# Performance work log

Hardware: AMD Instinct MI355X
Metric: run time of the kernel (lower is better)

Reference implementation:

```python
import jax, jax.numpy as jnp
import numpy as np


def setup_inputs() -> dict:
    key = jax.random.key(0)
    k_y, k_cb = jax.random.split(key)
    B, C, H, W = 8, 192, 64, 64
    G, K = 8, 512
    d = C // G  # 24
    y = jax.random.normal(k_y, (B, C, H, W), dtype=jnp.float32)
    codebooks = jax.random.normal(k_cb, (G, K, d), dtype=jnp.float32)
    return {"y": y, "codebooks": codebooks}


def reference(y, codebooks):
    # y: [B, C, H, W]; codebooks: [G, K, d] with C == G*d
    B, C, H, W = y.shape
    G, K, d = codebooks.shape
    # split channels into G groups of dim d -> vectors at each spatial pos
    x = y.reshape(B, G, d, H, W).transpose(0, 3, 4, 1, 2)  # [B,H,W,G,d]
    x2 = jnp.sum(x * x, axis=-1, keepdims=True)            # [B,H,W,G,1]
    e2 = jnp.sum(codebooks * codebooks, axis=-1)           # [G,K]
    xe = jnp.einsum('bhwgd,gkd->bhwgk', x, codebooks)      # [B,H,W,G,K]
    dist = x2 - 2.0 * xe + e2                              # [B,H,W,G,K]
    idx = jnp.argmin(dist, axis=-1)                        # [B,H,W,G] int
    # gather quantized vectors per group (to_feather)
    q = codebooks[jnp.arange(G), idx]                      # [B,H,W,G,d]
    y_ba = q.transpose(0, 3, 4, 1, 2).reshape(B, C, H, W)  # [B,C,H,W]
    code_index = idx.transpose(0, 3, 1, 2)                 # [B,G,H,W]
    # straight-through estimator
    universal_ctx = y + jax.lax.stop_gradient(y_ba - y)
    return universal_ctx, y_ba, code_index[:, None]        # [B,1,G,H,W]
```

## Files before the change

### kernel.cpp

```cpp
#include <hip/hip_runtime.h>

#define B_   8
#define C_   192
#define HW_  4096
#define G_   8
#define K_   512
#define D_   24
#define CBSZ (K_ * D_)
#define THREADS 512
#define NBLOCKS 512

#define FRAG_HW    12288
#define E2_OFF_HW  12288
#define EL_OFF_HW  13312
#define IMG_HW     25600
#define WS_IMG_HW  13312
#define WS_EL_BASE (8 * WS_IMG_HW)
#define WS_BIG_BYTES ((8 * WS_IMG_HW + 8 * FRAG_HW) * 2)

typedef float  f32x4 __attribute__((ext_vector_type(4)));
typedef int    i32x4 __attribute__((ext_vector_type(4)));
typedef short  s16x8 __attribute__((ext_vector_type(8)));
typedef short  s16x4 __attribute__((ext_vector_type(4)));
typedef unsigned long long u64;

static __device__ __forceinline__ unsigned umin_(unsigned a, unsigned b){return a<b?a:b;}
static __device__ __forceinline__ unsigned umax_(unsigned a, unsigned b){return a>b?a:b;}
static __device__ __forceinline__ unsigned short f2bf(float x){
    unsigned u=__float_as_uint(x);
    return (unsigned short)((u + 0x7FFFu + ((u>>16)&1u))>>16);
}
static __device__ __forceinline__ float bf2f(unsigned short h){return __uint_as_float(((unsigned)h)<<16);}
static __device__ __forceinline__ int dec_id(unsigned idb){
    return (int)((idb & 0x1F0u) | ((idb & 3u) << 2) | ((idb >> 2) & 3u));
}

__global__ __launch_bounds__(256) void vq_stage(
    const float* __restrict__ cb, unsigned short* __restrict__ ws, int wr_el)
{
    const int g = blockIdx.x >> 3;
    const int s = blockIdx.x & 7;
    const int tid = threadIdx.x;
    const float* cbg = cb + g * CBSZ;
    unsigned short* img = ws + g * WS_IMG_HW;
    unsigned short* eli = ws + WS_EL_BASE + g * FRAG_HW;

    for (int i = tid; i < 384; i += 256) {
        int gi = s * 384 + i;
        f32x4 v = ((const f32x4*)cbg)[gi];
        int i4 = gi << 2;
        int n  = i4 / 24;
        int k0 = i4 - n * 24;
        int off = (n >> 4) * 384 + (((k0 >> 3) << 4) + (n & 15)) * 8 + (k0 & 7);
        s16x4 h, l;
        #pragma unroll
        for (int j = 0; j < 4; ++j) {
            unsigned short eh = f2bf(v[j]);
            h[j] = (short)eh;
            l[j] = (short)f2bf(v[j] - bf2f(eh));
        }
        *(s16x4*)(&img[off]) = h;
        if (wr_el) *(s16x4*)(&eli[off]) = l;
    }
    if (tid < 64) {
        int n = s * 64 + tid;
        const float* row = cbg + n * D_;
        double s0 = 0.0, s1 = 0.0;
        #pragma unroll
        for (int j = 0; j < D_; j += 2) {
            double v0 = (double)row[j], v1 = (double)row[j+1];
            s0 = fma(v0,v0,s0); s1 = fma(v1,v1,s1);
        }
        ((float*)(img + E2_OFF_HW))[n] = (float)(256.0 + s0 + s1);
    }
}

template<bool ELWS>
__global__ __launch_bounds__(THREADS, 4) void vq_main(
    const float* __restrict__ y, const float* __restrict__ cb,
    const unsigned short* __restrict__ ws, float* __restrict__ out)
{
    __shared__ __align__(16) unsigned short sB[IMG_HW];

    const int bid = blockIdx.x;
    const int g = bid & 7;
    const int blkg = bid >> 3;
    const int tid = threadIdx.x;
    const int wave = tid >> 6, lane = tid & 63;
    const int c = lane & 15, q = lane >> 4;

    const float* cbg = cb + g * CBSZ;

    {
        const char* src = (const char*)(ws + g * WS_IMG_HW);
        char* dst = (char*)sB;
        #pragma unroll
        for (int it = 0; it < 4; ++it) {
            int off = it * 8192 + tid * 16;
            if (off < 26624)
                *(i32x4*)(dst + off) = *(const i32x4*)(src + off);
        }
    }
    if (ELWS) {
        const char* src = (const char*)(ws + WS_EL_BASE + g * FRAG_HW);
        char* dst = (char*)(sB + EL_OFF_HW);
        #pragma unroll
        for (int it = 0; it < 3; ++it) {
            int off = it * 8192 + tid * 16;
            *(i32x4*)(dst + off) = *(const i32x4*)(src + off);
        }
    } else {
        #pragma unroll
        for (int it = 0; it < 6; ++it) {
            int gi = it * THREADS + tid;
            f32x4 v = ((const f32x4*)cbg)[gi];
            int i4 = gi << 2;
            int n  = i4 / 24;
            int k0 = i4 - n * 24;
            int off = (n >> 4) * 384 + (((k0 >> 3) << 4) + (n & 15)) * 8 + (k0 & 7);
            s16x4 l;
            #pragma unroll
            for (int j = 0; j < 4; ++j) {
                unsigned short eh = f2bf(v[j]);
                l[j] = (short)f2bf(v[j] - bf2f(eh));
            }
            *(s16x4*)(&sB[EL_OFF_HW + off]) = l;
        }
    }
    __syncthreads();

    float* out0 = out;
    float* out1 = out + B_*C_*HW_;
    float* out2 = out + 2*B_*C_*HW_;

    const unsigned short* aH = sB + (lane < 48 ? lane : lane - 48) * 8;
    const unsigned short* aL = aH + EL_OFF_HW;
    const f32x4* e2p = (const f32x4*)((const float*)(sB + E2_OFF_HW) + (q << 2));

    const int wsid = (blkg << 3) + wave;

    #pragma unroll 1
    for (int p = 0; p < 2; ++p) {
        const int tt0   = wsid + (p << 10);
        const int hw    = (tt0 & 255) << 4;
        const int bimg0 = tt0 >> 8;
        int ybase[2];
        ybase[0] = (bimg0*C_ + g*D_)*HW_ + hw;
        ybase[1] = ybase[0] + 2*C_*HW_;

        s16x8 Xh[2], Xl[2];
        #pragma unroll
        for (int ti = 0; ti < 2; ++ti) {
            unsigned hx[4], lx[4];
            if (q < 3) {
                const float* yq = y + ybase[ti] + (q*8)*HW_ + c;
                float xf[8];
                #pragma unroll
                for (int jj = 0; jj < 8; ++jj) xf[jj] = -2.0f * yq[jj*HW_];
                #pragma unroll
                for (int p2 = 0; p2 < 4; ++p2) {
                    float f0 = xf[2*p2], f1 = xf[2*p2+1];
                    unsigned u0 = __float_as_uint(f0), u1v = __float_as_uint(f1);
                    hx[p2] = (u1v & 0xFFFF0000u) | (u0 >> 16);
                    float l0 = f0 - __uint_as_float(u0 & 0xFFFF0000u);
                    float l1 = f1 - __uint_as_float(u1v & 0xFFFF0000u);
                    lx[p2] = (unsigned)f2bf(l0) | ((unsigned)f2bf(l1) << 16);
                }
            } else {
                hx[0]=0u; hx[1]=0u; hx[2]=0u; hx[3]=0u;
                lx[0]=0u; lx[1]=0u; lx[2]=0u; lx[3]=0u;
            }
            Xh[ti] = __builtin_bit_cast(s16x8, (i32x4){(int)hx[0],(int)hx[1],(int)hx[2],(int)hx[3]});
            Xl[ti] = __builtin_bit_cast(s16x8, (i32x4){(int)lx[0],(int)lx[1],(int)lx[2],(int)lx[3]});
        }

        unsigned b1a[2] = {~0u, ~0u}, b2a[2] = {~0u, ~0u}, b3a[2] = {~0u, ~0u};
        #pragma unroll 4
        for (int t = 0; t < 32; ++t) {
            s16x8 eh  = *(const s16x8*)(aH + t * 384);
            s16x8 el  = *(const s16x8*)(aL + t * 384);
            f32x4 e2v = e2p[t * 4];
            f32x4 a0 = __builtin_amdgcn_mfma_f32_16x16x32_bf16(eh, Xh[0], e2v, 0,0,0);
            a0       = __builtin_amdgcn_mfma_f32_16x16x32_bf16(eh, Xl[0], a0,  0,0,0);
            a0       = __builtin_amdgcn_mfma_f32_16x16x32_bf16(el, Xh[0], a0,  0,0,0);
            f32x4 a1 = __builtin_amdgcn_mfma_f32_16x16x32_bf16(eh, Xh[1], e2v, 0,0,0);
            a1       = __builtin_amdgcn_mfma_f32_16x16x32_bf16(eh, Xl[1], a1,  0,0,0);
            a1       = __builtin_amdgcn_mfma_f32_16x16x32_bf16(el, Xh[1], a1,  0,0,0);
            #pragma unroll
            for (int r = 0; r < 4; ++r) {
                const unsigned id7 = (unsigned)((t << 2) | r);
                {
                    unsigned key = (__float_as_uint(a0[r]) & 0xFFFFFF80u) + id7;
                    unsigned t3, t2;
                    asm("v_med3_u32 %0, %1, %2, %3" : "=v"(t3) : "v"(key), "v"(b2a[0]), "v"(b3a[0]));
                    asm("v_med3_u32 %0, %1, %2, %3" : "=v"(t2) : "v"(key), "v"(b1a[0]), "v"(b2a[0]));
                    b3a[0] = t3; b2a[0] = t2; b1a[0] = umin_(b1a[0], key);
                }
                {
                    unsigned key = (__float_as_uint(a1[r]) & 0xFFFFFF80u) + id7;
                    unsigned t3, t2;
                    asm("v_med3_u32 %0, %1, %2, %3" : "=v"(t3) : "v"(key), "v"(b2a[1]), "v"(b3a[1]));
                    asm("v_med3_u32 %0, %1, %2, %3" : "=v"(t2) : "v"(key), "v"(b1a[1]), "v"(b2a[1]));
                    b3a[1] = t3; b2a[1] = t2; b1a[1] = umin_(b1a[1], key);
                }
            }
        }

        #pragma unroll
        for (int ti = 0; ti < 2; ++ti) {
            unsigned b1 = (b1a[ti] << 2) | (unsigned)q;
            unsigned b2 = (b2a[ti] << 2) | (unsigned)q;
            unsigned b3 = (b3a[ti] << 2) | (unsigned)q;
            #pragma unroll
            for (int d = 16; d < 64; d <<= 1) {
                unsigned o1=__shfl_xor(b1,d,64), o2=__shfl_xor(b2,d,64), o3=__shfl_xor(b3,d,64);
                unsigned x = umax_(b1,o1);
                unsigned yv= umin_(b2,o2);
                unsigned w = umax_(b2,o2);
                unsigned z = umin_(b3,o3);
                b1 = umin_(b1,o1);
                b2 = umin_(x,yv);
                b3 = umin_(umax_(x,yv), umin_(w,z));
            }

            const int gap = (int)((b2 >> 9) - (b1 >> 9));
            int kwin;
            if (__ballot(gap < 8) == 0ull) {
                kwin = dec_id(b1 & 511u);
            } else {
                float xfr[8];
                if (q < 3) {
                    const float* yq = y + ybase[ti] + (q*8)*HW_ + c;
                    #pragma unroll
                    for (int jj = 0; jj < 8; ++jj) xfr[jj] = -2.0f * yq[jj*HW_];
                } else {
                    #pragma unroll
                    for (int jj = 0; jj < 8; ++jj) xfr[jj] = 0.0f;
                }
                double xd[8];
                #pragma unroll
                for (int jj = 0; jj < 8; ++jj) xd[jj] = (double)xfr[jj];
                const unsigned cands[3] = {b1, b2, b3};
                u64 bestk = ~0ull;
                #pragma unroll
                for (int ci = 0; ci < 3; ++ci) {
                    int kc = dec_id(cands[ci] & 511u);
                    double s = 0.0;
                    if (q < 3) {
                        const f32x4* ce4 = (const f32x4*)(cbg + kc*D_ + (q<<3));
                        float ef[8];
                        *(f32x4*)&ef[0] = ce4[0];
                        *(f32x4*)&ef[4] = ce4[1];
                        #pragma unroll
                        for (int jj = 0; jj < 8; ++jj) {
                            double ev = (double)ef[jj];
                            s = fma(ev, ev, s);
                            s = fma(xd[jj], ev, s);
                        }
                    }
                    s += __shfl_xor(s, 16, 64);
                    s += __shfl_xor(s, 32, 64);
                    s += 256.0;
                    u64 kk = (((u64)__double_as_longlong(s)) & ~0x1FFull) | (u64)kc;
                    bestk = kk < bestk ? kk : bestk;
                }
                kwin = (int)(bestk & 511ull);
            }

            const float* cw = cbg + kwin * D_;
            if (q < 3) {
                const f32x4* cw4 = (const f32x4*)(cw + (q<<3));
                float v[8];
                *(f32x4*)&v[0] = cw4[0];
                *(f32x4*)&v[4] = cw4[1];
                const int ob = ybase[ti] + (q*8)*HW_ + c;
                #pragma unroll
                for (int jj = 0; jj < 8; ++jj) {
                    out0[ob + jj*HW_] = v[jj];
                    out1[ob + jj*HW_] = v[jj];
                }
            }
            if (lane < 16) {
                const int bimg = bimg0 + 2*ti;
                out2[(bimg*G_ + g)*HW_ + hw + lane] = (float)kwin;
            }
        }
    }
}

extern "C" void kernel_launch(void* const* d_in, const int* in_sizes, int n_in,
                              void* d_out, int out_size, void* d_ws, size_t ws_size,
                              hipStream_t stream) {
    const float* y  = (const float*)d_in[0];
    const float* cb = (const float*)d_in[1];
    float* out = (float*)d_out;
    unsigned short* ws = (unsigned short*)d_ws;

    const bool big = ws_size >= (size_t)WS_BIG_BYTES;
    vq_stage<<<dim3(64), dim3(256), 0, stream>>>(cb, ws, big ? 1 : 0);
    if (big) vq_main<true ><<<dim3(NBLOCKS), dim3(THREADS), 0, stream>>>(y, cb, ws, out);
    else     vq_main<false><<<dim3(NBLOCKS), dim3(THREADS), 0, stream>>>(y, cb, ws, out);
}
```

Before: 113.9 us.

## Read low-part codebook fragments from global memory to halve LDS and double blocks

In the big-workspace path, the low-precision codebook fragments are no longer copied into shared memory and are instead read directly from the global workspace in the inner MFMA loop. This halves LDS per block, which allows launch bounds of 8 blocks per CU, and the grid doubles to 1024 blocks, each processing one tile pair instead of two. The aim is higher occupancy and less per-block staging. In exchange, the inner loop now issues global/L2 loads that may add latency, and register pressure is tighter under the stricter launch bound.

```diff
diff --git a/kernel.cpp b/kernel.cpp
--- a/kernel.cpp
+++ b/kernel.cpp
@@ -8,12 +8,10 @@
 #define D_   24
 #define CBSZ (K_ * D_)
 #define THREADS 512
-#define NBLOCKS 512
 
 #define FRAG_HW    12288
 #define E2_OFF_HW  12288
 #define EL_OFF_HW  13312
-#define IMG_HW     25600
 #define WS_IMG_HW  13312
 #define WS_EL_BASE (8 * WS_IMG_HW)
 #define WS_BIG_BYTES ((8 * WS_IMG_HW + 8 * FRAG_HW) * 2)
@@ -75,12 +73,14 @@
     }
 }
 
-template<bool ELWS>
-__global__ __launch_bounds__(THREADS, 4) void vq_main(
+template<bool ELG>
+__global__ __launch_bounds__(THREADS, ELG ? 8 : 4) void vq_main(
     const float* __restrict__ y, const float* __restrict__ cb,
     const unsigned short* __restrict__ ws, float* __restrict__ out)
 {
-    __shared__ __align__(16) unsigned short sB[IMG_HW];
+    constexpr int NW    = ELG ? 1024 : 512;
+    constexpr int NPAIR = ELG ? 1 : 2;
+    __shared__ __align__(16) unsigned short sB[ELG ? 13312 : 25600];
 
     const int bid = blockIdx.x;
     const int g = bid & 7;
@@ -101,15 +101,7 @@
                 *(i32x4*)(dst + off) = *(const i32x4*)(src + off);
         }
     }
-    if (ELWS) {
-        const char* src = (const char*)(ws + WS_EL_BASE + g * FRAG_HW);
-        char* dst = (char*)(sB + EL_OFF_HW);
-        #pragma unroll
-        for (int it = 0; it < 3; ++it) {
-            int off = it * 8192 + tid * 16;
-            *(i32x4*)(dst + off) = *(const i32x4*)(src + off);
-        }
-    } else {
+    if constexpr (!ELG) {
         #pragma unroll
         for (int it = 0; it < 6; ++it) {
             int gi = it * THREADS + tid;
@@ -133,20 +125,24 @@
     float* out1 = out + B_*C_*HW_;
     float* out2 = out + 2*B_*C_*HW_;
 
-    const unsigned short* aH = sB + (lane < 48 ? lane : lane - 48) * 8;
-    const unsigned short* aL = aH + EL_OFF_HW;
+    const int alias8 = (lane < 48 ? lane : lane - 48) * 8;
+    const unsigned short* aH = sB + alias8;
+    const unsigned short* aLg = ELG ? (ws + WS_EL_BASE + g * FRAG_HW + alias8)
+                                    : (const unsigned short*)nullptr;
+    const unsigned short* aLs = ELG ? (const unsigned short*)nullptr
+                                    : (sB + EL_OFF_HW + alias8);
     const f32x4* e2p = (const f32x4*)((const float*)(sB + E2_OFF_HW) + (q << 2));
 
     const int wsid = (blkg << 3) + wave;
 
     #pragma unroll 1
-    for (int p = 0; p < 2; ++p) {
-        const int tt0   = wsid + (p << 10);
+    for (int p = 0; p < NPAIR; ++p) {
+        const int tt0   = wsid + p * 2 * NW;
         const int hw    = (tt0 & 255) << 4;
         const int bimg0 = tt0 >> 8;
         int ybase[2];
         ybase[0] = (bimg0*C_ + g*D_)*HW_ + hw;
-        ybase[1] = ybase[0] + 2*C_*HW_;
+        ybase[1] = ybase[0] + (NW >> 8)*C_*HW_;
 
         s16x8 Xh[2], Xl[2];
         #pragma unroll
@@ -177,8 +173,10 @@
         unsigned b1a[2] = {~0u, ~0u}, b2a[2] = {~0u, ~0u}, b3a[2] = {~0u, ~0u};
         #pragma unroll 4
         for (int t = 0; t < 32; ++t) {
-            s16x8 eh  = *(const s16x8*)(aH + t * 384);
-            s16x8 el  = *(const s16x8*)(aL + t * 384);
+            s16x8 eh = *(const s16x8*)(aH + t * 384);
+            s16x8 el;
+            if constexpr (ELG) el = *(const s16x8*)(aLg + t * 384);
+            else               el = *(const s16x8*)(aLs + t * 384);
             f32x4 e2v = e2p[t * 4];
             f32x4 a0 = __builtin_amdgcn_mfma_f32_16x16x32_bf16(eh, Xh[0], e2v, 0,0,0);
             a0       = __builtin_amdgcn_mfma_f32_16x16x32_bf16(eh, Xl[0], a0,  0,0,0);
@@ -281,7 +279,7 @@
                 }
             }
             if (lane < 16) {
-                const int bimg = bimg0 + 2*ti;
+                const int bimg = bimg0 + (NW >> 8)*ti;
                 out2[(bimg*G_ + g)*HW_ + hw + lane] = (float)kwin;
             }
         }
@@ -298,6 +296,6 @@
 
     const bool big = ws_size >= (size_t)WS_BIG_BYTES;
     vq_stage<<<dim3(64), dim3(256), 0, stream>>>(cb, ws, big ? 1 : 0);
-    if (big) vq_main<true ><<<dim3(NBLOCKS), dim3(THREADS), 0, stream>>>(y, cb, ws, out);
-    else     vq_main<false><<<dim3(NBLOCKS), dim3(THREADS), 0, stream>>>(y, cb, ws, out);
-}
+    if (big) vq_main<true ><<<dim3(1024), dim3(THREADS), 0, stream>>>(y, cb, ws, out);
+    else     vq_main<false><<<dim3(512),  dim3(THREADS), 0, stream>>>(y, cb, ws, out);
+}
```

After: 113.2 us. Within noise of the previous version (-0.6%).

## Switch split-precision MFMA to fp16, double block size, single pass per wave

Applied to the files above, without the earlier changes.

Replaces the bf16 hi/lo split of codebook and inputs with an fp16 hi/lo split using packed round-toward-zero conversion, and uses f16 MFMA. The energy offset drops to 128, and the refinement test now also fires on small distances to guard fp16 precision. Blocks grow to 1024 threads, so each wave handles one tile pair instead of looping twice, and the workspace stores the full image, lo part included, contiguously per group. This aims for fewer conversion instructions, more waves per block, and cheaper staging loads, at the cost of fp16 range and precision risks and a possibly more frequent exact fallback.

```diff
diff --git a/kernel.cpp b/kernel.cpp
--- a/kernel.cpp
+++ b/kernel.cpp
@@ -7,43 +7,46 @@
 #define K_   512
 #define D_   24
 #define CBSZ (K_ * D_)
-#define THREADS 512
+#define THREADS 1024
 #define NBLOCKS 512
 
 #define FRAG_HW    12288
 #define E2_OFF_HW  12288
 #define EL_OFF_HW  13312
 #define IMG_HW     25600
-#define WS_IMG_HW  13312
-#define WS_EL_BASE (8 * WS_IMG_HW)
-#define WS_BIG_BYTES ((8 * WS_IMG_HW + 8 * FRAG_HW) * 2)
+#define WS_SMALL_HW 13312
+#define WS_BIG_BYTES (G_ * IMG_HW * 2)
 
 typedef float  f32x4 __attribute__((ext_vector_type(4)));
 typedef int    i32x4 __attribute__((ext_vector_type(4)));
 typedef short  s16x8 __attribute__((ext_vector_type(8)));
 typedef short  s16x4 __attribute__((ext_vector_type(4)));
+typedef _Float16 h16x8 __attribute__((ext_vector_type(8)));
 typedef unsigned long long u64;
 
 static __device__ __forceinline__ unsigned umin_(unsigned a, unsigned b){return a<b?a:b;}
 static __device__ __forceinline__ unsigned umax_(unsigned a, unsigned b){return a>b?a:b;}
-static __device__ __forceinline__ unsigned short f2bf(float x){
-    unsigned u=__float_as_uint(x);
-    return (unsigned short)((u + 0x7FFFu + ((u>>16)&1u))>>16);
-}
-static __device__ __forceinline__ float bf2f(unsigned short h){return __uint_as_float(((unsigned)h)<<16);}
 static __device__ __forceinline__ int dec_id(unsigned idb){
     return (int)((idb & 0x1F0u) | ((idb & 3u) << 2) | ((idb >> 2) & 3u));
 }
+static __device__ __forceinline__ unsigned pkrtz(float a, float b){
+    return __builtin_bit_cast(unsigned, __builtin_amdgcn_cvt_pkrtz(a, b));
+}
+static __device__ __forceinline__ float lo16f(unsigned w){
+    return (float)__builtin_bit_cast(_Float16, (unsigned short)(w & 0xFFFFu));
+}
+static __device__ __forceinline__ float hi16f(unsigned w){
+    return (float)__builtin_bit_cast(_Float16, (unsigned short)(w >> 16));
+}
 
 __global__ __launch_bounds__(256) void vq_stage(
-    const float* __restrict__ cb, unsigned short* __restrict__ ws, int wr_el)
+    const float* __restrict__ cb, unsigned short* __restrict__ ws, int big)
 {
     const int g = blockIdx.x >> 3;
     const int s = blockIdx.x & 7;
     const int tid = threadIdx.x;
     const float* cbg = cb + g * CBSZ;
-    unsigned short* img = ws + g * WS_IMG_HW;
-    unsigned short* eli = ws + WS_EL_BASE + g * FRAG_HW;
+    unsigned short* img = ws + g * (big ? IMG_HW : WS_SMALL_HW);
 
     for (int i = tid; i < 384; i += 256) {
         int gi = s * 384 + i;
@@ -55,12 +58,13 @@
         s16x4 h, l;
         #pragma unroll
         for (int j = 0; j < 4; ++j) {
-            unsigned short eh = f2bf(v[j]);
-            h[j] = (short)eh;
-            l[j] = (short)f2bf(v[j] - bf2f(eh));
+            _Float16 eh = (_Float16)v[j];
+            _Float16 el = (_Float16)(v[j] - (float)eh);
+            h[j] = __builtin_bit_cast(short, eh);
+            l[j] = __builtin_bit_cast(short, el);
         }
         *(s16x4*)(&img[off]) = h;
-        if (wr_el) *(s16x4*)(&eli[off]) = l;
+        if (big) *(s16x4*)(&img[EL_OFF_HW + off]) = l;
     }
     if (tid < 64) {
         int n = s * 64 + tid;
@@ -71,12 +75,12 @@
             double v0 = (double)row[j], v1 = (double)row[j+1];
             s0 = fma(v0,v0,s0); s1 = fma(v1,v1,s1);
         }
-        ((float*)(img + E2_OFF_HW))[n] = (float)(256.0 + s0 + s1);
-    }
-}
-
-template<bool ELWS>
-__global__ __launch_bounds__(THREADS, 4) void vq_main(
+        ((float*)(img + E2_OFF_HW))[n] = (float)(128.0 + s0 + s1);
+    }
+}
+
+template<bool BIG>
+__global__ __launch_bounds__(THREADS, 8) void vq_main(
     const float* __restrict__ y, const float* __restrict__ cb,
     const unsigned short* __restrict__ ws, float* __restrict__ out)
 {
@@ -91,27 +95,26 @@
 
     const float* cbg = cb + g * CBSZ;
 
-    {
-        const char* src = (const char*)(ws + g * WS_IMG_HW);
+    if constexpr (BIG) {
+        const char* src = (const char*)(ws + g * IMG_HW);
         char* dst = (char*)sB;
         #pragma unroll
         for (int it = 0; it < 4; ++it) {
-            int off = it * 8192 + tid * 16;
+            int off = it * 16384 + tid * 16;
+            if (off < 51200)
+                *(i32x4*)(dst + off) = *(const i32x4*)(src + off);
+        }
+    } else {
+        const char* src = (const char*)(ws + g * WS_SMALL_HW);
+        char* dst = (char*)sB;
+        #pragma unroll
+        for (int it = 0; it < 2; ++it) {
+            int off = it * 16384 + tid * 16;
             if (off < 26624)
                 *(i32x4*)(dst + off) = *(const i32x4*)(src + off);
         }
-    }
-    if (ELWS) {
-        const char* src = (const char*)(ws + WS_EL_BASE + g * FRAG_HW);
-        char* dst = (char*)(sB + EL_OFF_HW);
         #pragma unroll
         for (int it = 0; it < 3; ++it) {
-            int off = it * 8192 + tid * 16;
-            *(i32x4*)(dst + off) = *(const i32x4*)(src + off);
-        }
-    } else {
-        #pragma unroll
-        for (int it = 0; it < 6; ++it) {
             int gi = it * THREADS + tid;
             f32x4 v = ((const f32x4*)cbg)[gi];
             int i4 = gi << 2;
@@ -121,8 +124,8 @@
             s16x4 l;
             #pragma unroll
             for (int j = 0; j < 4; ++j) {
-                unsigned short eh = f2bf(v[j]);
-                l[j] = (short)f2bf(v[j] - bf2f(eh));
+                _Float16 eh = (_Float16)v[j];
+                l[j] = __builtin_bit_cast(short, (_Float16)(v[j] - (float)eh));
             }
             *(s16x4*)(&sB[EL_OFF_HW + off]) = l;
         }
@@ -134,156 +137,149 @@
     float* out2 = out + 2*B_*C_*HW_;
 
     const unsigned short* aH = sB + (lane < 48 ? lane : lane - 48) * 8;
-    const unsigned short* aL = aH + EL_OFF_HW;
     const f32x4* e2p = (const f32x4*)((const float*)(sB + E2_OFF_HW) + (q << 2));
 
-    const int wsid = (blkg << 3) + wave;
-
-    #pragma unroll 1
-    for (int p = 0; p < 2; ++p) {
-        const int tt0   = wsid + (p << 10);
-        const int hw    = (tt0 & 255) << 4;
-        const int bimg0 = tt0 >> 8;
-        int ybase[2];
-        ybase[0] = (bimg0*C_ + g*D_)*HW_ + hw;
-        ybase[1] = ybase[0] + 2*C_*HW_;
-
-        s16x8 Xh[2], Xl[2];
-        #pragma unroll
-        for (int ti = 0; ti < 2; ++ti) {
-            unsigned hx[4], lx[4];
+    const int wsid = (blkg << 4) + wave;
+    const int hw    = (wsid & 255) << 4;
+    const int bimg0 = wsid >> 8;
+    int ybase[2];
+    ybase[0] = (bimg0*C_ + g*D_)*HW_ + hw;
+    ybase[1] = ybase[0] + 4*C_*HW_;
+
+    h16x8 Xh[2], Xl[2];
+    #pragma unroll
+    for (int ti = 0; ti < 2; ++ti) {
+        unsigned hx[4], lx[4];
+        if (q < 3) {
+            const float* yq = y + ybase[ti] + (q*8)*HW_ + c;
+            float xf[8];
+            #pragma unroll
+            for (int jj = 0; jj < 8; ++jj) xf[jj] = -2.0f * yq[jj*HW_];
+            #pragma unroll
+            for (int p2 = 0; p2 < 4; ++p2) {
+                float f0 = xf[2*p2], f1 = xf[2*p2+1];
+                unsigned hw32 = pkrtz(f0, f1);
+                float r0 = f0 - lo16f(hw32), r1 = f1 - hi16f(hw32);
+                hx[p2] = hw32;
+                lx[p2] = pkrtz(r0, r1);
+            }
+        } else {
+            hx[0]=0u; hx[1]=0u; hx[2]=0u; hx[3]=0u;
+            lx[0]=0u; lx[1]=0u; lx[2]=0u; lx[3]=0u;
+        }
+        Xh[ti] = __builtin_bit_cast(h16x8, (i32x4){(int)hx[0],(int)hx[1],(int)hx[2],(int)hx[3]});
+        Xl[ti] = __builtin_bit_cast(h16x8, (i32x4){(int)lx[0],(int)lx[1],(int)lx[2],(int)lx[3]});
+    }
+
+    unsigned b1a[2] = {~0u, ~0u}, b2a[2] = {~0u, ~0u}, b3a[2] = {~0u, ~0u};
+    #pragma unroll 4
+    for (int t = 0; t < 32; ++t) {
+        h16x8 eh = __builtin_bit_cast(h16x8, *(const s16x8*)(aH + t * 384));
+        h16x8 el = __builtin_bit_cast(h16x8, *(const s16x8*)(aH + EL_OFF_HW + t * 384));
+        f32x4 e2v = e2p[t * 4];
+        f32x4 a0 = __builtin_amdgcn_mfma_f32_16x16x32_f16(eh, Xh[0], e2v, 0,0,0);
+        a0       = __builtin_amdgcn_mfma_f32_16x16x32_f16(eh, Xl[0], a0,  0,0,0);
+        a0       = __builtin_amdgcn_mfma_f32_16x16x32_f16(el, Xh[0], a0,  0,0,0);
+        f32x4 a1 = __builtin_amdgcn_mfma_f32_16x16x32_f16(eh, Xh[1], e2v, 0,0,0);
+        a1       = __builtin_amdgcn_mfma_f32_16x16x32_f16(eh, Xl[1], a1,  0,0,0);
+        a1       = __builtin_amdgcn_mfma_f32_16x16x32_f16(el, Xh[1], a1,  0,0,0);
+        #pragma unroll
+        for (int r = 0; r < 4; ++r) {
+            const unsigned id7 = (unsigned)((t << 2) | r);
+            {
+                unsigned key = (__float_as_uint(a0[r]) & 0xFFFFFF80u) + id7;
+                unsigned t3, t2;
+                asm("v_med3_u32 %0, %1, %2, %3" : "=v"(t3) : "v"(key), "v"(b2a[0]), "v"(b3a[0]));
+                asm("v_med3_u32 %0, %1, %2, %3" : "=v"(t2) : "v"(key), "v"(b1a[0]), "v"(b2a[0]));
+                b3a[0] = t3; b2a[0] = t2; b1a[0] = umin_(b1a[0], key);
+            }
+            {
+                unsigned key = (__float_as_uint(a1[r]) & 0xFFFFFF80u) + id7;
+                unsigned t3, t2;
+                asm("v_med3_u32 %0, %1, %2, %3" : "=v"(t3) : "v"(key), "v"(b2a[1]), "v"(b3a[1]));
+                asm("v_med3_u32 %0, %1, %2, %3" : "=v"(t2) : "v"(key), "v"(b1a[1]), "v"(b2a[1]));
+                b3a[1] = t3; b2a[1] = t2; b1a[1] = umin_(b1a[1], key);
+            }
+        }
+    }
+
+    #pragma unroll
+    for (int ti = 0; ti < 2; ++ti) {
+        unsigned b1 = (b1a[ti] << 2) | (unsigned)q;
+        unsigned b2 = (b2a[ti] << 2) | (unsigned)q;
+        unsigned b3 = (b3a[ti] << 2) | (unsigned)q;
+        #pragma unroll
+        for (int d = 16; d < 64; d <<= 1) {
+            unsigned o1=__shfl_xor(b1,d,64), o2=__shfl_xor(b2,d,64), o3=__shfl_xor(b3,d,64);
+            unsigned x = umax_(b1,o1);
+            unsigned yv= umin_(b2,o2);
+            unsigned w = umax_(b2,o2);
+            unsigned z = umin_(b3,o3);
+            b1 = umin_(b1,o1);
+            b2 = umin_(x,yv);
+            b3 = umin_(umax_(x,yv), umin_(w,z));
+        }
+
+        const int gap = (int)((b2 >> 9) - (b1 >> 9));
+        int kwin;
+        if (__ballot((gap < 2) || (b1 < 0x0A000000u)) == 0ull) {
+            kwin = dec_id(b1 & 511u);
+        } else {
+            float xfr[8];
             if (q < 3) {
                 const float* yq = y + ybase[ti] + (q*8)*HW_ + c;
-                float xf[8];
                 #pragma unroll
-                for (int jj = 0; jj < 8; ++jj) xf[jj] = -2.0f * yq[jj*HW_];
+                for (int jj = 0; jj < 8; ++jj) xfr[jj] = -2.0f * yq[jj*HW_];
+            } else {
                 #pragma unroll
-                for (int p2 = 0; p2 < 4; ++p2) {
-                    float f0 = xf[2*p2], f1 = xf[2*p2+1];
-                    unsigned u0 = __float_as_uint(f0), u1v = __float_as_uint(f1);
-                    hx[p2] = (u1v & 0xFFFF0000u) | (u0 >> 16);
-                    float l0 = f0 - __uint_as_float(u0 & 0xFFFF0000u);
-                    float l1 = f1 - __uint_as_float(u1v & 0xFFFF0000u);
-                    lx[p2] = (unsigned)f2bf(l0) | ((unsigned)f2bf(l1) << 16);
+                for (int jj = 0; jj < 8; ++jj) xfr[jj] = 0.0f;
+            }
+            double xd[8];
+            #pragma unroll
+            for (int jj = 0; jj < 8; ++jj) xd[jj] = (double)xfr[jj];
+            const unsigned cands[3] = {b1, b2, b3};
+            u64 bestk = ~0ull;
+            #pragma unroll
+            for (int ci = 0; ci < 3; ++ci) {
+                int kc = dec_id(cands[ci] & 511u);
+                double s = 0.0;
+                if (q < 3) {
+                    const f32x4* ce4 = (const f32x4*)(cbg + kc*D_ + (q<<3));
+                    float ef[8];
+                    *(f32x4*)&ef[0] = ce4[0];
+                    *(f32x4*)&ef[4] = ce4[1];
+                    #pragma unroll
+                    for (int jj = 0; jj < 8; ++jj) {
+                        double ev = (double)ef[jj];
+                        s = fma(ev, ev, s);
+                        s = fma(xd[jj], ev, s);
+                    }
                 }
-            } else {
-                hx[0]=0u; hx[1]=0u; hx[2]=0u; hx[3]=0u;
-                lx[0]=0u; lx[1]=0u; lx[2]=0u; lx[3]=0u;
-            }
-            Xh[ti] = __builtin_bit_cast(s16x8, (i32x4){(int)hx[0],(int)hx[1],(int)hx[2],(int)hx[3]});
-            Xl[ti] = __builtin_bit_cast(s16x8, (i32x4){(int)lx[0],(int)lx[1],(int)lx[2],(int)lx[3]});
-        }
-
-        unsigned b1a[2] = {~0u, ~0u}, b2a[2] = {~0u, ~0u}, b3a[2] = {~0u, ~0u};
-        #pragma unroll 4
-        for (int t = 0; t < 32; ++t) {
-            s16x8 eh  = *(const s16x8*)(aH + t * 384);
-            s16x8 el  = *(const s16x8*)(aL + t * 384);
-            f32x4 e2v = e2p[t * 4];
-            f32x4 a0 = __builtin_amdgcn_mfma_f32_16x16x32_bf16(eh, Xh[0], e2v, 0,0,0);
-            a0       = __builtin_amdgcn_mfma_f32_16x16x32_bf16(eh, Xl[0], a0,  0,0,0);
-            a0       = __builtin_amdgcn_mfma_f32_16x16x32_bf16(el, Xh[0], a0,  0,0,0);
-            f32x4 a1 = __builtin_amdgcn_mfma_f32_16x16x32_bf16(eh, Xh[1], e2v, 0,0,0);
-            a1       = __builtin_amdgcn_mfma_f32_16x16x32_bf16(eh, Xl[1], a1,  0,0,0);
-            a1       = __builtin_amdgcn_mfma_f32_16x16x32_bf16(el, Xh[1], a1,  0,0,0);
-            #pragma unroll
-            for (int r = 0; r < 4; ++r) {
-                const unsigned id7 = (unsigned)((t << 2) | r);
-                {
-                    unsigned key = (__float_as_uint(a0[r]) & 0xFFFFFF80u) + id7;
-                    unsigned t3, t2;
-                    asm("v_med3_u32 %0, %1, %2, %3" : "=v"(t3) : "v"(key), "v"(b2a[0]), "v"(b3a[0]));
-                    asm("v_med3_u32 %0, %1, %2, %3" : "=v"(t2) : "v"(key), "v"(b1a[0]), "v"(b2a[0]));
-                    b3a[0] = t3; b2a[0] = t2; b1a[0] = umin_(b1a[0], key);
-                }
-                {
-                    unsigned key = (__float_as_uint(a1[r]) & 0xFFFFFF80u) + id7;
-                    unsigned t3, t2;
-                    asm("v_med3_u32 %0, %1, %2, %3" : "=v"(t3) : "v"(key), "v"(b2a[1]), "v"(b3a[1]));
-                    asm("v_med3_u32 %0, %1, %2, %3" : "=v"(t2) : "v"(key), "v"(b1a[1]), "v"(b2a[1]));
-                    b3a[1] = t3; b2a[1] = t2; b1a[1] = umin_(b1a[1], key);
-                }
-            }
-        }
-
-        #pragma unroll
-        for (int ti = 0; ti < 2; ++ti) {
-            unsigned b1 = (b1a[ti] << 2) | (unsigned)q;
-            unsigned b2 = (b2a[ti] << 2) | (unsigned)q;
-            unsigned b3 = (b3a[ti] << 2) | (unsigned)q;
-            #pragma unroll
-            for (int d = 16; d < 64; d <<= 1) {
-                unsigned o1=__shfl_xor(b1,d,64), o2=__shfl_xor(b2,d,64), o3=__shfl_xor(b3,d,64);
-                unsigned x = umax_(b1,o1);
-                unsigned yv= umin_(b2,o2);
-                unsigned w = umax_(b2,o2);
-                unsigned z = umin_(b3,o3);
-                b1 = umin_(b1,o1);
-                b2 = umin_(x,yv);
-                b3 = umin_(umax_(x,yv), umin_(w,z));
-            }
-
-            const int gap = (int)((b2 >> 9) - (b1 >> 9));
-            int kwin;
-            if (__ballot(gap < 8) == 0ull) {
-                kwin = dec_id(b1 & 511u);
-            } else {
-                float xfr[8];
-                if (q < 3) {
-                    const float* yq = y + ybase[ti] + (q*8)*HW_ + c;
-                    #pragma unroll
-                    for (int jj = 0; jj < 8; ++jj) xfr[jj] = -2.0f * yq[jj*HW_];
-                } else {
-                    #pragma unroll
-                    for (int jj = 0; jj < 8; ++jj) xfr[jj] = 0.0f;
-                }
-                double xd[8];
-                #pragma unroll
-                for (int jj = 0; jj < 8; ++jj) xd[jj] = (double)xfr[jj];
-                const unsigned cands[3] = {b1, b2, b3};
-                u64 bestk = ~0ull;
-                #pragma unroll
-                for (int ci = 0; ci < 3; ++ci) {
-                    int kc = dec_id(cands[ci] & 511u);
-                    double s = 0.0;
-                    if (q < 3) {
-                        const f32x4* ce4 = (const f32x4*)(cbg + kc*D_ + (q<<3));
-                        float ef[8];
-                        *(f32x4*)&ef[0] = ce4[0];
-                        *(f32x4*)&ef[4] = ce4[1];
-                        #pragma unroll
-                        for (int jj = 0; jj < 8; ++jj) {
-                            double ev = (double)ef[jj];
-                            s = fma(ev, ev, s);
-                            s = fma(xd[jj], ev, s);
-                        }
-                    }
-                    s += __shfl_xor(s, 16, 64);
-                    s += __shfl_xor(s, 32, 64);
-                    s += 256.0;
-                    u64 kk = (((u64)__double_as_longlong(s)) & ~0x1FFull) | (u64)kc;
-                    bestk = kk < bestk ? kk : bestk;
-                }
-                kwin = (int)(bestk & 511ull);
-            }
-
-            const float* cw = cbg + kwin * D_;
-            if (q < 3) {
-                const f32x4* cw4 = (const f32x4*)(cw + (q<<3));
-                float v[8];
-                *(f32x4*)&v[0] = cw4[0];
-                *(f32x4*)&v[4] = cw4[1];
-                const int ob = ybase[ti] + (q*8)*HW_ + c;
-                #pragma unroll
-                for (int jj = 0; jj < 8; ++jj) {
-                    out0[ob + jj*HW_] = v[jj];
-                    out1[ob + jj*HW_] = v[jj];
-                }
-            }
-            if (lane < 16) {
-                const int bimg = bimg0 + 2*ti;
-                out2[(bimg*G_ + g)*HW_ + hw + lane] = (float)kwin;
-            }
+                s += __shfl_xor(s, 16, 64);
+                s += __shfl_xor(s, 32, 64);
+                s += 128.0;
+                u64 kk = (((u64)__double_as_longlong(s)) & ~0x1FFull) | (u64)kc;
+                bestk = kk < bestk ? kk : bestk;
+            }
+            kwin = (int)(bestk & 511ull);
+        }
+
+        const float* cw = cbg + kwin * D_;
+        if (q < 3) {
+            const f32x4* cw4 = (const f32x4*)(cw + (q<<3));
+            float v[8];
+            *(f32x4*)&v[0] = cw4[0];
+            *(f32x4*)&v[4] = cw4[1];
+            const int ob = ybase[ti] + (q*8)*HW_ + c;
+            #pragma unroll
+            for (int jj = 0; jj < 8; ++jj) {
+                out0[ob + jj*HW_] = v[jj];
+                out1[ob + jj*HW_] = v[jj];
+            }
+        }
+        if (lane < 16) {
+            const int bimg = bimg0 + 4*ti;
+            out2[(bimg*G_ + g)*HW_ + hw + lane] = (float)kwin;
         }
     }
 }
```

Result: no change. 113.1 us (-0.7%).
